# Kernel tuning notes

Hardware: AMD Instinct MI355X
Metric: run time of the kernel (lower is better)

The kernel has to match this reference:

```python
import jax, jax.numpy as jnp
import numpy as np

# Dims: N tokens, D=in_features, E experts, H=head_size, K=top-k, EMB=embed_dim
N, D, E, H, K, EMB = 65536, 256, 4, 512, 2, 512


def setup_inputs() -> dict:
    key = jax.random.key(0)
    ks = jax.random.split(key, 6)
    s_d = 1.0 / np.sqrt(D)
    s_h = 1.0 / np.sqrt(H)
    return {
        "x": jax.random.normal(ks[0], (N, D), jnp.float32),
        "w_gate": jax.random.normal(ks[1], (D, E), jnp.float32) * s_d,   # gating linear
        "w1": jax.random.normal(ks[2], (E, D, H), jnp.float32) * s_d,    # expert up-proj
        "w2": jax.random.normal(ks[3], (E, H, D), jnp.float32) * s_h,    # expert down-proj
        "w_proj": jax.random.normal(ks[4], (D, EMB), jnp.float32) * s_d, # final nn.Linear weight (in, out)
        "b_proj": jnp.zeros((EMB,), jnp.float32),
    }


def reference(x, w_gate, w1, w2, w_proj, b_proj):
    # --- top-k gating (eval mode: no gating noise) ---
    logits = x @ w_gate                                   # [N, E]
    top_logits, top_idx = jax.lax.top_k(logits, K)        # [N, K]
    top_gates = jax.nn.softmax(top_logits, axis=-1)       # softmax over the k selected logits
    n_idx = jnp.arange(x.shape[0])[:, None]
    gates = jnp.zeros_like(logits).at[n_idx, top_idx].set(top_gates)  # dense sparse-gate matrix [N, E]

    # --- expert compute + combine (dense-masked equivalent of dispatch/scatter) ---
    h = jax.nn.gelu(jnp.einsum('nd,edh->neh', x, w1), approximate=False)  # [N, E, H]
    y = jnp.einsum('neh,ehd,ne->nd', h, w2, gates)                         # [N, D]

    # --- output projection ---
    return y @ w_proj + b_proj                            # [N, EMB]
```

## Files before the change

### kernel.cpp

```cpp
#include <hip/hip_runtime.h>
#include <hip/hip_bf16.h>
#include <math.h>


typedef __attribute__((ext_vector_type(4))) float f32x4;
typedef __attribute__((ext_vector_type(8))) short bf16x8;
typedef unsigned int u32;

#define MFMA16(a, b, c) __builtin_amdgcn_mfma_f32_16x16x32_bf16((a), (b), (c), 0, 0, 0)

#define WAITVM4() asm volatile("s_waitcnt vmcnt(4)" ::: "memory")
#define WAITVM2() asm volatile("s_waitcnt vmcnt(2)" ::: "memory")
#define WAITVM0() asm volatile("s_waitcnt vmcnt(0)" ::: "memory")
#define WAITLG0() asm volatile("s_waitcnt lgkmcnt(0)" ::: "memory")
#define SBAR() do { __builtin_amdgcn_sched_barrier(0); \
                    __builtin_amdgcn_s_barrier(); \
                    __builtin_amdgcn_sched_barrier(0); } while (0)
#define GLDS16(g, l) __builtin_amdgcn_global_load_lds( \
    (const __attribute__((address_space(1))) u32*)(g), \
    (__attribute__((address_space(3))) u32*)(l), 16, 0, 0)

__device__ __forceinline__ float bf2f(__hip_bfloat16 v) { return __bfloat162float(v); }

__device__ __forceinline__ float gelu_f(float v) {
    float t = 0.7978845608028654f * v * (1.f + 0.044715f * v * v);
    float e = __expf(2.f * t);
    float th = 1.f - 2.f * __builtin_amdgcn_rcpf(e + 1.f);
    return 0.5f * v * (1.f + th);
}

__global__ void k_sniff(const unsigned short* __restrict__ xr, int* __restrict__ flag) {
    int lane = threadIdx.x;
    int cnt = 0;
#pragma unroll
    for (int j = 0; j < 4; ++j) {
        unsigned short v = xr[2 * (lane * 4 + j)];
        int e = (v >> 7) & 0xFF;
        cnt += (e >= 97 && e <= 157) ? 1 : 0;
    }
#pragma unroll
    for (int off = 32; off; off >>= 1) cnt += __shfl_down(cnt, off);
    if (lane == 0) flag[0] = (cnt < 192) ? 1 : 0;
}

__global__ void k_prep(const void* __restrict__ w1,
                       const void* __restrict__ w2,
                       const void* __restrict__ wp,
                       const int* __restrict__ flag,
                       char* __restrict__ stream) {
    int G = blockIdx.x * 256 + threadIdx.x;
    int s = G >> 10, q = G & 1023;
    const bool f32m = (flag[0] != 0);
    const void* W;
    int srcBase, stride, dpos;
    if (s < 128) {
        int e = s >> 5, r = s & 31, hci = r >> 3, stl = r & 7;
        if (stl < 4) {
            int row = q & 127, gpos = q >> 7;
            int g = gpos ^ (row & 7);
            int h = hci * 128 + row;
            int kb = stl * 64 + g * 8;
            W = w1; srcBase = (e << 17) + (kb << 9) + h; stride = 512;
            dpos = (s << 14) + row * 128 + gpos * 16;
        } else {
            int row = q & 255, gpos = q >> 8;
            int g = gpos ^ ((row >> 1) & 3);
            int hb = hci * 128 + (stl - 4) * 32 + g * 8;
            W = w2; srcBase = (e << 17) + (hb << 8) + row; stride = 256;
            dpos = (s << 14) + row * 64 + gpos * 16;
        }
    } else {
        int ps = s - 128;
        int row = q & 255, gpos = q >> 8;
        int g = gpos ^ ((row >> 1) & 3);
        int n = (ps >> 3) * 256 + row;
        int kb = (ps & 7) * 32 + g * 8;
        W = wp; srcBase = (kb << 9) + n; stride = 512;
        dpos = (s << 14) + row * 64 + gpos * 16;
    }
    union { unsigned short u[8]; uint4 v; } o;
#pragma unroll
    for (int j = 0; j < 8; ++j) {
        int si = srcBase + j * stride;
        if (f32m) {
            union { __hip_bfloat16 b; unsigned short u; } c;
            c.b = __float2bfloat16(((const float*)W)[si]);
            o.u[j] = c.u;
        } else {
            o.u[j] = ((const unsigned short*)W)[si];
        }
    }
    *(uint4*)(stream + dpos) = o.v;
}

__global__ __launch_bounds__(512, 2) void k_moe(
    const void* __restrict__ xin,
    const void* __restrict__ wg,
    const char* __restrict__ stream,
    const void* __restrict__ bp,
    const int* __restrict__ flag,
    void* __restrict__ outp) {
    extern __shared__ char smem[];
    __hip_bfloat16* Xs = (__hip_bfloat16*)smem;
    __hip_bfloat16* Hs = (__hip_bfloat16*)(smem + 67584);
    float* gate_s = (float*)(smem + 102400);
    float* wgs = (float*)(smem + 67584);
    __hip_bfloat16* Ys = (__hip_bfloat16*)smem;
    char* ring = smem;
    char* pring = smem + 67584;

    const int tid = threadIdx.x;
    const int m0 = blockIdx.x * 128;
    const bool f32m = (flag[0] != 0);

    if (!f32m) {
        const uint4* xg = (const uint4*)((const __hip_bfloat16*)xin + (size_t)m0 * 256);
#pragma unroll
        for (int i = 0; i < 8; ++i) {
            int f = tid + 512 * i;
            int r = f >> 5, c = f & 31;
            *(uint4*)&Xs[r * 264 + c * 8] = xg[f];
        }
    } else {
        const float4* xg = (const float4*)((const float*)xin + (size_t)m0 * 256);
#pragma unroll
        for (int i = 0; i < 8; ++i) {
            int f = tid + 512 * i;
            int r = f >> 5, c = f & 31;
            float4 a = xg[2 * f], b = xg[2 * f + 1];
            __hip_bfloat16* d = &Xs[r * 264 + c * 8];
            d[0] = __float2bfloat16(a.x); d[1] = __float2bfloat16(a.y);
            d[2] = __float2bfloat16(a.z); d[3] = __float2bfloat16(a.w);
            d[4] = __float2bfloat16(b.x); d[5] = __float2bfloat16(b.y);
            d[6] = __float2bfloat16(b.z); d[7] = __float2bfloat16(b.w);
        }
    }
    if (tid < 256) {
#pragma unroll
        for (int e = 0; e < 4; ++e)
            wgs[e * 256 + tid] = f32m ? ((const float*)wg)[tid * 4 + e]
                                      : bf2f(((const __hip_bfloat16*)wg)[tid * 4 + e]);
    }
    __syncthreads();

    {
        int tok = tid >> 2, ge = tid & 3;
        float acc = 0.f;
        if (f32m) {
            const float4* xrow = (const float4*)((const float*)xin + (size_t)(m0 + tok) * 256);
            const float* wrow = &wgs[ge * 256];
#pragma unroll 8
            for (int qd = 0; qd < 64; ++qd) {
                float4 xv = xrow[qd];
                acc += xv.x * wrow[qd * 4] + xv.y * wrow[qd * 4 + 1]
                     + xv.z * wrow[qd * 4 + 2] + xv.w * wrow[qd * 4 + 3];
            }
        } else {
            const float* wrow = &wgs[ge * 256];
#pragma unroll 4
            for (int d8 = 0; d8 < 32; ++d8) {
                bf16x8 xv = *(const bf16x8*)&Xs[tok * 264 + d8 * 8];
#pragma unroll
                for (int j = 0; j < 8; ++j) {
                    union { unsigned u; float f; } c;
                    c.u = ((unsigned)(unsigned short)xv[j]) << 16;
                    acc += c.f * wrow[d8 * 8 + j];
                }
            }
        }
        gate_s[tok * 4 + ge] = acc;
    }
    __syncthreads();
    if (tid < 128) {
        float l[4];
#pragma unroll
        for (int e = 0; e < 4; ++e) l[e] = gate_s[tid * 4 + e];
        int i0 = 0; float v0 = l[0];
#pragma unroll
        for (int e = 1; e < 4; ++e)
            if (l[e] > v0) { v0 = l[e]; i0 = e; }
        int i1 = -1; float v1 = -1e30f;
#pragma unroll
        for (int e = 0; e < 4; ++e)
            if (e != i0 && l[e] > v1) { v1 = l[e]; i1 = e; }
        float t = __expf(v1 - v0);
        float g0 = 1.f / (1.f + t);
        float g1 = t * g0;
#pragma unroll
        for (int e = 0; e < 4; ++e) gate_s[tid * 4 + e] = 0.f;
        gate_s[tid * 4 + i0] = g0;
        gate_s[tid * 4 + i1] = g1;
    }
    __syncthreads();

    const int lane = tid & 63;
    const int wv = tid >> 6;
    const int wr = wv & 3;
    const int wc = wv >> 2;
    const int lm = lane & 15, quad = lane >> 4;
    const int swzB = quad ^ ((lm >> 1) & 3);

    bf16x8 ax[2][8];
#pragma unroll
    for (int mt = 0; mt < 2; ++mt)
#pragma unroll
        for (int ks = 0; ks < 8; ++ks)
            ax[mt][ks] = *(const bf16x8*)&Xs[(32 * wr + 16 * mt + lm) * 264 + ks * 32 + quad * 8];
    __syncthreads();

    const char* src_base = stream + tid * 16;
    char* dst_base = ring + ((tid >> 6) << 10);

    {
        const char* s0 = src_base; char* d0 = dst_base;
        GLDS16(s0, d0); GLDS16(s0 + 8192, d0 + 8192);
        const char* s1 = src_base + 16384; char* d1 = dst_base + 16384;
        GLDS16(s1, d1); GLDS16(s1 + 8192, d1 + 8192);
    }

    f32x4 Yacc[2][8];
#pragma unroll
    for (int a = 0; a < 2; ++a)
#pragma unroll
        for (int b = 0; b < 8; ++b) Yacc[a][b] = (f32x4){0.f, 0.f, 0.f, 0.f};

    int sidx = 0;
#pragma unroll 1
    for (int e = 0; e < 4; ++e) {
#pragma unroll 1
        for (int hci = 0; hci < 4; ++hci) {
            f32x4 Hacc[2][4];
#pragma unroll
            for (int a = 0; a < 2; ++a)
#pragma unroll
                for (int b = 0; b < 4; ++b) Hacc[a][b] = (f32x4){0.f, 0.f, 0.f, 0.f};
#pragma unroll
            for (int stA = 0; stA < 4; ++stA) {
                int nxt = sidx + 2;
                if (nxt < 128) {
                    const char* sp = src_base + ((size_t)nxt << 14);
                    char* dp = dst_base + ((nxt & 3) << 14);
                    GLDS16(sp, dp); GLDS16(sp + 8192, dp + 8192);
                    WAITVM4();
                } else if (nxt == 128) WAITVM2(); else WAITVM0();
                SBAR();
                const char* rb = ring + ((sidx & 3) << 14);
#pragma unroll
                for (int ks = 0; ks < 2; ++ks)
#pragma unroll
                    for (int nt = 0; nt < 4; ++nt) {
                        int row = 64 * wc + 16 * nt + lm;
                        bf16x8 b = *(const bf16x8*)(rb + row * 128
                                      + ((((ks << 2) | quad) ^ (lm & 7)) << 4));
                        Hacc[0][nt] = MFMA16(ax[0][2 * stA + ks], b, Hacc[0][nt]);
                        Hacc[1][nt] = MFMA16(ax[1][2 * stA + ks], b, Hacc[1][nt]);
                    }
                ++sidx;
                if (stA == 3) {
#pragma unroll
                    for (int mt = 0; mt < 2; ++mt)
#pragma unroll
                        for (int nt = 0; nt < 4; ++nt)
#pragma unroll
                            for (int r = 0; r < 4; ++r) {
                                int row = 32 * wr + 16 * mt + quad * 4 + r;
                                int col = 64 * wc + 16 * nt + lm;
                                float g = gelu_f(Hacc[mt][nt][r]) * gate_s[row * 4 + e];
                                Hs[row * 136 + col] = __float2bfloat16(g);
                            }
                    WAITLG0();
                }
            }
#pragma unroll
            for (int stB = 0; stB < 4; ++stB) {
                int nxt = sidx + 2;
                if (nxt < 128) {
                    const char* sp = src_base + ((size_t)nxt << 14);
                    char* dp = dst_base + ((nxt & 3) << 14);
                    GLDS16(sp, dp); GLDS16(sp + 8192, dp + 8192);
                    WAITVM4();
                } else if (nxt == 128) WAITVM2(); else WAITVM0();
                SBAR();
                const char* rb = ring + ((sidx & 3) << 14);
                bf16x8 af0 = *(const bf16x8*)&Hs[(32 * wr + lm) * 136 + stB * 32 + quad * 8];
                bf16x8 af1 = *(const bf16x8*)&Hs[(32 * wr + 16 + lm) * 136 + stB * 32 + quad * 8];
#pragma unroll
                for (int nt = 0; nt < 8; ++nt) {
                    int row = 128 * wc + 16 * nt + lm;
                    bf16x8 b = *(const bf16x8*)(rb + row * 64 + (swzB << 4));
                    Yacc[0][nt] = MFMA16(af0, b, Yacc[0][nt]);
                    Yacc[1][nt] = MFMA16(af1, b, Yacc[1][nt]);
                }
                ++sidx;
            }
        }
    }

    SBAR();
    {
        const char* s0 = stream + ((size_t)128 << 14) + tid * 16;
        char* d0 = pring + ((tid >> 6) << 10);
        GLDS16(s0, d0); GLDS16(s0 + 8192, d0 + 8192);
        const char* s1 = s0 + 16384; char* d1 = d0 + 16384;
        GLDS16(s1, d1); GLDS16(s1 + 8192, d1 + 8192);
    }
#pragma unroll
    for (int mt = 0; mt < 2; ++mt)
#pragma unroll
        for (int nt = 0; nt < 8; ++nt)
#pragma unroll
            for (int r = 0; r < 4; ++r) {
                int row = 32 * wr + 16 * mt + quad * 4 + r;
                int col = 128 * wc + 16 * nt + lm;
                Ys[row * 260 + col] = __float2bfloat16(Yacc[mt][nt][r]);
            }
    WAITLG0();
    WAITVM2();
    SBAR();

    f32x4 Pacc[2][8];
#pragma unroll
    for (int a = 0; a < 2; ++a)
#pragma unroll
        for (int b = 0; b < 8; ++b) Pacc[a][b] = (f32x4){0.f, 0.f, 0.f, 0.f};
#pragma unroll 1
    for (int ps = 0; ps < 16; ++ps) {
        if (ps > 0) {
            SBAR();
            if (ps < 15) {
                const char* sp = stream + ((size_t)(129 + ps) << 14) + tid * 16;
                char* dp = pring + (((ps + 1) & 1) << 14) + ((tid >> 6) << 10);
                GLDS16(sp, dp); GLDS16(sp + 8192, dp + 8192);
                WAITVM2();
            } else WAITVM0();
            SBAR();
        }
        int t = ps & 7;
        const char* pb = pring + ((ps & 1) << 14);
        bf16x8 af0 = *(const bf16x8*)&Ys[(32 * wr + lm) * 260 + t * 32 + quad * 8];
        bf16x8 af1 = *(const bf16x8*)&Ys[(32 * wr + 16 + lm) * 260 + t * 32 + quad * 8];
#pragma unroll
        for (int nt = 0; nt < 8; ++nt) {
            int row = 128 * wc + 16 * nt + lm;
            bf16x8 b = *(const bf16x8*)(pb + row * 64 + (swzB << 4));
            Pacc[0][nt] = MFMA16(af0, b, Pacc[0][nt]);
            Pacc[1][nt] = MFMA16(af1, b, Pacc[1][nt]);
        }
        if (t == 7) {
            int p = ps >> 3;
#pragma unroll
            for (int nt = 0; nt < 8; ++nt) {
                int col = 256 * p + 128 * wc + 16 * nt + lm;
                float bv = f32m ? ((const float*)bp)[col] : bf2f(((const __hip_bfloat16*)bp)[col]);
#pragma unroll
                for (int mt = 0; mt < 2; ++mt)
#pragma unroll
                    for (int r = 0; r < 4; ++r) {
                        int row = m0 + 32 * wr + 16 * mt + quad * 4 + r;
                        float v = Pacc[mt][nt][r] + bv;
                        if (f32m) ((float*)outp)[(size_t)row * 512 + col] = v;
                        else ((__hip_bfloat16*)outp)[(size_t)row * 512 + col] = __float2bfloat16(v);
                    }
            }
            if (ps < 15) {
#pragma unroll
                for (int a = 0; a < 2; ++a)
#pragma unroll
                    for (int b = 0; b < 8; ++b) Pacc[a][b] = (f32x4){0.f, 0.f, 0.f, 0.f};
            }
        }
    }
}

extern "C" void kernel_launch(void* const* d_in, const int* in_sizes, int n_in,
                              void* d_out, int out_size, void* d_ws, size_t ws_size,
                              hipStream_t stream) {
    const void* x  = d_in[0];
    const void* wg = d_in[1];
    const void* w1 = d_in[2];
    const void* w2 = d_in[3];
    const void* wp = d_in[4];
    const void* bp = d_in[5];

    char* ws = (char*)d_ws;
    int* flag = (int*)(ws + 0);
    char* wstream = ws + 4096;

    k_sniff<<<1, 64, 0, stream>>>((const unsigned short*)x, flag);
    k_prep<<<576, 256, 0, stream>>>(w1, w2, wp, flag, wstream);
    k_moe<<<512, 512, 104448, stream>>>(x, wg, wstream, bp, flag, d_out);
}
```

Before: 409.4 us.

## Halve MoE block tile, use triple-buffered weight ring, and inline dtype sniff

```diff
diff --git a/kernel.cpp b/kernel.cpp
--- a/kernel.cpp
+++ b/kernel.cpp
@@ -10,7 +10,6 @@
 #define MFMA16(a, b, c) __builtin_amdgcn_mfma_f32_16x16x32_bf16((a), (b), (c), 0, 0, 0)
 
 #define WAITVM4() asm volatile("s_waitcnt vmcnt(4)" ::: "memory")
-#define WAITVM2() asm volatile("s_waitcnt vmcnt(2)" ::: "memory")
 #define WAITVM0() asm volatile("s_waitcnt vmcnt(0)" ::: "memory")
 #define WAITLG0() asm volatile("s_waitcnt lgkmcnt(0)" ::: "memory")
 #define SBAR() do { __builtin_amdgcn_sched_barrier(0); \
@@ -22,35 +21,24 @@
 
 __device__ __forceinline__ float bf2f(__hip_bfloat16 v) { return __bfloat162float(v); }
 
-__device__ __forceinline__ float gelu_f(float v) {
-    float t = 0.7978845608028654f * v * (1.f + 0.044715f * v * v);
-    float e = __expf(2.f * t);
-    float th = 1.f - 2.f * __builtin_amdgcn_rcpf(e + 1.f);
-    return 0.5f * v * (1.f + th);
-}
-
-__global__ void k_sniff(const unsigned short* __restrict__ xr, int* __restrict__ flag) {
-    int lane = threadIdx.x;
+__device__ __forceinline__ bool sniff_f32(const unsigned short* __restrict__ xr) {
     int cnt = 0;
 #pragma unroll
-    for (int j = 0; j < 4; ++j) {
-        unsigned short v = xr[2 * (lane * 4 + j)];
-        int e = (v >> 7) & 0xFF;
+    for (int j = 0; j < 32; ++j) {
+        int e = (xr[2 * j] >> 7) & 0xFF;
         cnt += (e >= 97 && e <= 157) ? 1 : 0;
     }
-#pragma unroll
-    for (int off = 32; off; off >>= 1) cnt += __shfl_down(cnt, off);
-    if (lane == 0) flag[0] = (cnt < 192) ? 1 : 0;
+    return cnt < 16;
 }
 
 __global__ void k_prep(const void* __restrict__ w1,
                        const void* __restrict__ w2,
                        const void* __restrict__ wp,
-                       const int* __restrict__ flag,
+                       const unsigned short* __restrict__ xr,
                        char* __restrict__ stream) {
     int G = blockIdx.x * 256 + threadIdx.x;
     int s = G >> 10, q = G & 1023;
-    const bool f32m = (flag[0] != 0);
+    const bool f32m = sniff_f32(xr);
     const void* W;
     int srcBase, stride, dpos;
     if (s < 128) {
@@ -93,31 +81,30 @@
     *(uint4*)(stream + dpos) = o.v;
 }
 
-__global__ __launch_bounds__(512, 2) void k_moe(
+__global__ __launch_bounds__(256, 2) void k_moe(
     const void* __restrict__ xin,
     const void* __restrict__ wg,
     const char* __restrict__ stream,
     const void* __restrict__ bp,
-    const int* __restrict__ flag,
     void* __restrict__ outp) {
     extern __shared__ char smem[];
     __hip_bfloat16* Xs = (__hip_bfloat16*)smem;
-    __hip_bfloat16* Hs = (__hip_bfloat16*)(smem + 67584);
-    float* gate_s = (float*)(smem + 102400);
-    float* wgs = (float*)(smem + 67584);
-    __hip_bfloat16* Ys = (__hip_bfloat16*)smem;
-    char* ring = smem;
-    char* pring = smem + 67584;
+    char* hsb = smem + 49152;
+    float* gate_s = (float*)(smem + 65536);
+    float* wgs = (float*)(smem + 36864);
+    char* ysb = smem;
+    char* peven = smem + 32768;
+    char* podd  = smem + 49152;
 
     const int tid = threadIdx.x;
-    const int m0 = blockIdx.x * 128;
-    const bool f32m = (flag[0] != 0);
+    const int m0 = blockIdx.x * 64;
+    const bool f32m = sniff_f32((const unsigned short*)xin);
 
     if (!f32m) {
         const uint4* xg = (const uint4*)((const __hip_bfloat16*)xin + (size_t)m0 * 256);
 #pragma unroll
         for (int i = 0; i < 8; ++i) {
-            int f = tid + 512 * i;
+            int f = tid + 256 * i;
             int r = f >> 5, c = f & 31;
             *(uint4*)&Xs[r * 264 + c * 8] = xg[f];
         }
@@ -125,7 +112,7 @@
         const float4* xg = (const float4*)((const float*)xin + (size_t)m0 * 256);
 #pragma unroll
         for (int i = 0; i < 8; ++i) {
-            int f = tid + 512 * i;
+            int f = tid + 256 * i;
             int r = f >> 5, c = f & 31;
             float4 a = xg[2 * f], b = xg[2 * f + 1];
             __hip_bfloat16* d = &Xs[r * 264 + c * 8];
@@ -135,7 +122,7 @@
             d[6] = __float2bfloat16(b.z); d[7] = __float2bfloat16(b.w);
         }
     }
-    if (tid < 256) {
+    {
 #pragma unroll
         for (int e = 0; e < 4; ++e)
             wgs[e * 256 + tid] = f32m ? ((const float*)wg)[tid * 4 + e]
@@ -171,7 +158,7 @@
         gate_s[tok * 4 + ge] = acc;
     }
     __syncthreads();
-    if (tid < 128) {
+    if (tid < 64) {
         float l[4];
 #pragma unroll
         for (int e = 0; e < 4; ++e) l[e] = gate_s[tid * 4 + e];
@@ -195,8 +182,8 @@
 
     const int lane = tid & 63;
     const int wv = tid >> 6;
-    const int wr = wv & 3;
-    const int wc = wv >> 2;
+    const int wr = wv & 1;
+    const int wc = wv >> 1;
     const int lm = lane & 15, quad = lane >> 4;
     const int swzB = quad ^ ((lm >> 1) & 3);
 
@@ -209,13 +196,15 @@
     __syncthreads();
 
     const char* src_base = stream + tid * 16;
-    char* dst_base = ring + ((tid >> 6) << 10);
+    const int woff = (tid >> 6) << 10;
 
     {
-        const char* s0 = src_base; char* d0 = dst_base;
-        GLDS16(s0, d0); GLDS16(s0 + 8192, d0 + 8192);
-        const char* s1 = src_base + 16384; char* d1 = dst_base + 16384;
-        GLDS16(s1, d1); GLDS16(s1 + 8192, d1 + 8192);
+        const char* s0 = src_base; char* d0 = smem + woff;
+        GLDS16(s0, d0); GLDS16(s0 + 4096, d0 + 4096);
+        GLDS16(s0 + 8192, d0 + 8192); GLDS16(s0 + 12288, d0 + 12288);
+        const char* s1 = src_base + 16384; char* d1 = smem + 16384 + woff;
+        GLDS16(s1, d1); GLDS16(s1 + 4096, d1 + 4096);
+        GLDS16(s1 + 8192, d1 + 8192); GLDS16(s1 + 12288, d1 + 12288);
     }
 
     f32x4 Yacc[2][8];
@@ -224,7 +213,7 @@
 #pragma unroll
         for (int b = 0; b < 8; ++b) Yacc[a][b] = (f32x4){0.f, 0.f, 0.f, 0.f};
 
-    int sidx = 0;
+    int sidx = 0, cur = 0;
 #pragma unroll 1
     for (int e = 0; e < 4; ++e) {
 #pragma unroll 1
@@ -236,26 +225,28 @@
                 for (int b = 0; b < 4; ++b) Hacc[a][b] = (f32x4){0.f, 0.f, 0.f, 0.f};
 #pragma unroll
             for (int stA = 0; stA < 4; ++stA) {
-                int nxt = sidx + 2;
-                if (nxt < 128) {
-                    const char* sp = src_base + ((size_t)nxt << 14);
-                    char* dp = dst_base + ((nxt & 3) << 14);
-                    GLDS16(sp, dp); GLDS16(sp + 8192, dp + 8192);
-                    WAITVM4();
-                } else if (nxt == 128) WAITVM2(); else WAITVM0();
+                WAITVM4();
                 SBAR();
-                const char* rb = ring + ((sidx & 3) << 14);
+                {
+                    int ns = cur + 2; if (ns >= 3) ns -= 3;
+                    const char* sp = src_base + ((size_t)(sidx + 2) << 14);
+                    char* dp = smem + ns * 16384 + woff;
+                    GLDS16(sp, dp); GLDS16(sp + 4096, dp + 4096);
+                    GLDS16(sp + 8192, dp + 8192); GLDS16(sp + 12288, dp + 12288);
+                }
+                const char* rb = smem + cur * 16384;
+                __builtin_amdgcn_s_setprio(1);
 #pragma unroll
                 for (int ks = 0; ks < 2; ++ks)
 #pragma unroll
                     for (int nt = 0; nt < 4; ++nt) {
-                        int row = 64 * wc + 16 * nt + lm;
-                        bf16x8 b = *(const bf16x8*)(rb + row * 128
+                        int rown = 64 * wc + 16 * nt + lm;
+                        bf16x8 b = *(const bf16x8*)(rb + rown * 128
                                       + ((((ks << 2) | quad) ^ (lm & 7)) << 4));
                         Hacc[0][nt] = MFMA16(ax[0][2 * stA + ks], b, Hacc[0][nt]);
                         Hacc[1][nt] = MFMA16(ax[1][2 * stA + ks], b, Hacc[1][nt]);
                     }
-                ++sidx;
+                __builtin_amdgcn_s_setprio(0);
                 if (stA == 3) {
 #pragma unroll
                     for (int mt = 0; mt < 2; ++mt)
@@ -265,33 +256,48 @@
                             for (int r = 0; r < 4; ++r) {
                                 int row = 32 * wr + 16 * mt + quad * 4 + r;
                                 int col = 64 * wc + 16 * nt + lm;
-                                float g = gelu_f(Hacc[mt][nt][r]) * gate_s[row * 4 + e];
-                                Hs[row * 136 + col] = __float2bfloat16(g);
+                                float v = Hacc[mt][nt][r];
+                                float vv = v * v;
+                                float w = fmaf(0.044715f, vv, 1.0f);
+                                float u = 1.5957691216f * v * w;
+                                float ex = __expf(u);
+                                float rr = __builtin_amdgcn_rcpf(ex + 1.0f);
+                                float vg = v * gate_s[row * 4 + e];
+                                float res = fmaf(-vg, rr, vg);
+                                *(__hip_bfloat16*)(hsb + row * 256
+                                    + ((col * 2) ^ ((row & 7) << 4))) = __float2bfloat16(res);
                             }
                     WAITLG0();
                 }
+                ++sidx; cur = (cur < 2) ? cur + 1 : 0;
             }
 #pragma unroll
             for (int stB = 0; stB < 4; ++stB) {
-                int nxt = sidx + 2;
-                if (nxt < 128) {
-                    const char* sp = src_base + ((size_t)nxt << 14);
-                    char* dp = dst_base + ((nxt & 3) << 14);
-                    GLDS16(sp, dp); GLDS16(sp + 8192, dp + 8192);
-                    WAITVM4();
-                } else if (nxt == 128) WAITVM2(); else WAITVM0();
+                if (sidx == 127) WAITVM0(); else WAITVM4();
                 SBAR();
-                const char* rb = ring + ((sidx & 3) << 14);
-                bf16x8 af0 = *(const bf16x8*)&Hs[(32 * wr + lm) * 136 + stB * 32 + quad * 8];
-                bf16x8 af1 = *(const bf16x8*)&Hs[(32 * wr + 16 + lm) * 136 + stB * 32 + quad * 8];
+                if (sidx + 2 <= 127) {
+                    int ns = cur + 2; if (ns >= 3) ns -= 3;
+                    const char* sp = src_base + ((size_t)(sidx + 2) << 14);
+                    char* dp = smem + ns * 16384 + woff;
+                    GLDS16(sp, dp); GLDS16(sp + 4096, dp + 4096);
+                    GLDS16(sp + 8192, dp + 8192); GLDS16(sp + 12288, dp + 12288);
+                }
+                const char* rb = smem + cur * 16384;
+                int r0 = 32 * wr + lm;
+                bf16x8 af0 = *(const bf16x8*)(hsb + r0 * 256
+                                + ((stB * 64 + quad * 16) ^ ((r0 & 7) << 4)));
+                bf16x8 af1 = *(const bf16x8*)(hsb + (r0 + 16) * 256
+                                + ((stB * 64 + quad * 16) ^ ((r0 & 7) << 4)));
+                __builtin_amdgcn_s_setprio(1);
 #pragma unroll
                 for (int nt = 0; nt < 8; ++nt) {
-                    int row = 128 * wc + 16 * nt + lm;
-                    bf16x8 b = *(const bf16x8*)(rb + row * 64 + (swzB << 4));
+                    int rown = 128 * wc + 16 * nt + lm;
+                    bf16x8 b = *(const bf16x8*)(rb + rown * 64 + (swzB << 4));
                     Yacc[0][nt] = MFMA16(af0, b, Yacc[0][nt]);
                     Yacc[1][nt] = MFMA16(af1, b, Yacc[1][nt]);
                 }
-                ++sidx;
+                __builtin_amdgcn_s_setprio(0);
+                ++sidx; cur = (cur < 2) ? cur + 1 : 0;
             }
         }
     }
@@ -299,10 +305,13 @@
     SBAR();
     {
         const char* s0 = stream + ((size_t)128 << 14) + tid * 16;
-        char* d0 = pring + ((tid >> 6) << 10);
-        GLDS16(s0, d0); GLDS16(s0 + 8192, d0 + 8192);
-        const char* s1 = s0 + 16384; char* d1 = d0 + 16384;
-        GLDS16(s1, d1); GLDS16(s1 + 8192, d1 + 8192);
+        char* d0 = peven + woff;
+        GLDS16(s0, d0); GLDS16(s0 + 4096, d0 + 4096);
+        GLDS16(s0 + 8192, d0 + 8192); GLDS16(s0 + 12288, d0 + 12288);
+        const char* s1 = stream + ((size_t)129 << 14) + tid * 16;
+        char* d1 = podd + woff;
+        GLDS16(s1, d1); GLDS16(s1 + 4096, d1 + 4096);
+        GLDS16(s1 + 8192, d1 + 8192); GLDS16(s1 + 12288, d1 + 12288);
     }
 #pragma unroll
     for (int mt = 0; mt < 2; ++mt)
@@ -312,10 +321,11 @@
             for (int r = 0; r < 4; ++r) {
                 int row = 32 * wr + 16 * mt + quad * 4 + r;
                 int col = 128 * wc + 16 * nt + lm;
-                Ys[row * 260 + col] = __float2bfloat16(Yacc[mt][nt][r]);
+                *(__hip_bfloat16*)(ysb + row * 512
+                    + ((col * 2) ^ ((row & 7) << 4))) = __float2bfloat16(Yacc[mt][nt][r]);
             }
     WAITLG0();
-    WAITVM2();
+    WAITVM4();
     SBAR();
 
     f32x4 Pacc[2][8];
@@ -329,23 +339,29 @@
             SBAR();
             if (ps < 15) {
                 const char* sp = stream + ((size_t)(129 + ps) << 14) + tid * 16;
-                char* dp = pring + (((ps + 1) & 1) << 14) + ((tid >> 6) << 10);
-                GLDS16(sp, dp); GLDS16(sp + 8192, dp + 8192);
-                WAITVM2();
+                char* dp = (((ps + 1) & 1) ? podd : peven) + woff;
+                GLDS16(sp, dp); GLDS16(sp + 4096, dp + 4096);
+                GLDS16(sp + 8192, dp + 8192); GLDS16(sp + 12288, dp + 12288);
+                WAITVM4();
             } else WAITVM0();
             SBAR();
         }
         int t = ps & 7;
-        const char* pb = pring + ((ps & 1) << 14);
-        bf16x8 af0 = *(const bf16x8*)&Ys[(32 * wr + lm) * 260 + t * 32 + quad * 8];
-        bf16x8 af1 = *(const bf16x8*)&Ys[(32 * wr + 16 + lm) * 260 + t * 32 + quad * 8];
+        const char* pb = (ps & 1) ? podd : peven;
+        int r0 = 32 * wr + lm;
+        bf16x8 af0 = *(const bf16x8*)(ysb + r0 * 512
+                        + ((t * 64 + quad * 16) ^ ((r0 & 7) << 4)));
+        bf16x8 af1 = *(const bf16x8*)(ysb + (r0 + 16) * 512
+                        + ((t * 64 + quad * 16) ^ ((r0 & 7) << 4)));
+        __builtin_amdgcn_s_setprio(1);
 #pragma unroll
         for (int nt = 0; nt < 8; ++nt) {
-            int row = 128 * wc + 16 * nt + lm;
-            bf16x8 b = *(const bf16x8*)(pb + row * 64 + (swzB << 4));
+            int rown = 128 * wc + 16 * nt + lm;
+            bf16x8 b = *(const bf16x8*)(pb + rown * 64 + (swzB << 4));
             Pacc[0][nt] = MFMA16(af0, b, Pacc[0][nt]);
             Pacc[1][nt] = MFMA16(af1, b, Pacc[1][nt]);
         }
+        __builtin_amdgcn_s_setprio(0);
         if (t == 7) {
             int p = ps >> 3;
 #pragma unroll
@@ -382,11 +398,8 @@
     const void* wp = d_in[4];
     const void* bp = d_in[5];
 
-    char* ws = (char*)d_ws;
-    int* flag = (int*)(ws + 0);
-    char* wstream = ws + 4096;
-
-    k_sniff<<<1, 64, 0, stream>>>((const unsigned short*)x, flag);
-    k_prep<<<576, 256, 0, stream>>>(w1, w2, wp, flag, wstream);
-    k_moe<<<512, 512, 104448, stream>>>(x, wg, wstream, bp, flag, d_out);
+    char* wstream = (char*)d_ws;
+
+    k_prep<<<576, 256, 0, stream>>>(w1, w2, wp, (const unsigned short*)x, wstream);
+    k_moe<<<1024, 256, 66560, stream>>>(x, wg, wstream, bp, d_out);
 }
```

New measurement: 386.2 us. -5.7%, faster.
